# Performance work log

Measured on AMD Instinct MI355X. Metric: run time of the kernel, lower is better.

Reference implementation:

```python
import jax, jax.numpy as jnp
import numpy as np

B, S, HID = 2, 2048, 1024
NH = 16
DK = HID // NH


def setup_inputs() -> dict:
    key0 = jax.random.key(0)
    ks = jax.random.split(key0, 16)
    inp = {
        "query": jax.random.normal(ks[0], (B, S, HID), dtype=jnp.float32),
        "key": jax.random.normal(ks[1], (B, S, HID), dtype=jnp.float32),
        "value": jax.random.normal(ks[2], (B, S, HID), dtype=jnp.float32),
        "bias": jax.random.uniform(ks[3], (B, S), dtype=jnp.float32),
        "mask": jax.random.randint(ks[4], (B, 1, S), 0, 2, dtype=jnp.int32),
        "wq": jax.random.normal(ks[5], (HID, HID), dtype=jnp.float32) * 0.02,
        "bq": jax.random.normal(ks[6], (HID,), dtype=jnp.float32) * 0.02,
        "wk": jax.random.normal(ks[7], (HID, HID), dtype=jnp.float32) * 0.02,
        "bk": jax.random.normal(ks[8], (HID,), dtype=jnp.float32) * 0.02,
        "wv": jax.random.normal(ks[9], (HID, HID), dtype=jnp.float32) * 0.02,
        "bv": jax.random.normal(ks[10], (HID,), dtype=jnp.float32) * 0.02,
        "wo": jax.random.normal(ks[11], (HID, HID), dtype=jnp.float32) * 0.02,
        "bo": jax.random.normal(ks[12], (HID,), dtype=jnp.float32) * 0.02,
    }
    return inp


def reference(query, key, value, bias, mask, wq, bq, wk, bk, wv, bv, wo, bo):
    b, s, hid = query.shape
    # attn_bias_type == 'both': gate K and V with per-token scalar bias
    # (dropout is eval-mode identity): x + p[..., None] * x
    key = key + bias[:, :, None] * key
    value = value + bias[:, :, None] * value

    def proj(x, w, bb):
        # torch Linear: x @ W.T + b, then split heads -> [b, nh, s, dk]
        y = x @ w.T + bb
        return y.reshape(b, s, NH, DK).transpose(0, 2, 1, 3)

    q = proj(query, wq, bq)
    k = proj(key, wk, bk)
    v = proj(value, wv, bv)

    scores = jnp.einsum("bhqd,bhkd->bhqk", q, k) / jnp.sqrt(jnp.asarray(DK, q.dtype))
    m = mask[:, None]  # [b,1,1,s] broadcast over heads and query positions
    scores = jnp.where(m == 0, jnp.asarray(-10000.0, scores.dtype), scores)
    p_attn = jax.nn.softmax(scores, axis=-1)
    x = jnp.einsum("bhqk,bhkd->bhqd", p_attn, v)
    x = x.transpose(0, 2, 1, 3).reshape(b, s, hid)
    return x @ wo.T + bo
```

## Files before the change

### kernel.cpp

```cpp
#include <hip/hip_runtime.h>
#include <stdint.h>

#define NB   2
#define SS   2048
#define HIDN 1024
#define NHEAD 16
#define DKK  64

typedef __attribute__((ext_vector_type(8))) short bf16x8;
typedef __attribute__((ext_vector_type(4))) float f32x4;

__device__ __forceinline__ uint16_t f2bf(float f) {
    uint32_t u = __float_as_uint(f);
    u += 0x7FFF + ((u >> 16) & 1);
    return (uint16_t)(u >> 16);
}
__device__ __forceinline__ uint32_t pk2(float f0, float f1) {
    uint32_t u0 = __float_as_uint(f0);
    uint32_t u1 = __float_as_uint(f1);
    u0 += 0x7FFF + ((u0 >> 16) & 1);
    u1 += 0x7FFF + ((u1 >> 16) & 1);
    return (u0 >> 16) | (u1 & 0xFFFF0000u);
}
__device__ __forceinline__ uint4 pack8(const float* __restrict__ s, float sc) {
    float4 a = *(const float4*)s;
    float4 b = *(const float4*)(s + 4);
    uint4 r;
    r.x = pk2(sc * a.x, sc * a.y);
    r.y = pk2(sc * a.z, sc * a.w);
    r.z = pk2(sc * b.x, sc * b.y);
    r.w = pk2(sc * b.z, sc * b.w);
    return r;
}
__device__ __forceinline__ void gl_lds16(const uint16_t* g, uint16_t* l) {
    __builtin_amdgcn_global_load_lds((const __attribute__((address_space(1))) void*)g,
                                     (__attribute__((address_space(3))) void*)l,
                                     16, 0, 0);
}

__global__ __launch_bounds__(256, 4)
void cvt_all(const float* __restrict__ q, const float* __restrict__ k,
             const float* __restrict__ v, const float* __restrict__ bias,
             const float* __restrict__ w0, const float* __restrict__ w1,
             const float* __restrict__ w2, const float* __restrict__ w3,
             uint16_t* __restrict__ q16, uint16_t* __restrict__ k16,
             uint16_t* __restrict__ v16, uint16_t* __restrict__ w16o)
{
    int i = blockIdx.x * 256 + threadIdx.x;
    if (i < 524288) {
        size_t e = (size_t)i * 8;
        float sc = 1.0f + bias[i >> 7];
        *(uint4*)(q16 + e) = pack8(q + e, 1.0f);
        *(uint4*)(k16 + e) = pack8(k + e, sc);
        *(uint4*)(v16 + e) = pack8(v + e, sc);
    } else {
        int j = i - 524288;
        const float* src = (j < 131072) ? w0 : (j < 262144) ? w1
                         : (j < 393216) ? w2 : w3;
        size_t e = (size_t)(j & 131071) * 8;
        *(uint4*)(w16o + (size_t)(j >> 17) * 1048576 + e) = pack8(src + e, 1.0f);
    }
}

__device__ __forceinline__ void gemm_core(const uint16_t* __restrict__ A,
                                          const uint16_t* __restrict__ W,
                                          uint16_t* __restrict__ As0,
                                          uint16_t* __restrict__ As1,
                                          uint16_t* __restrict__ Bs0,
                                          uint16_t* __restrict__ Bs1,
                                          int m0, int n0,
                                          f32x4 acc[4][2])
{
    const int t    = threadIdx.x;
    const int w    = t >> 6;
    const int lane = t & 63;
    const int q    = lane >> 4;
    const int lr   = lane & 15;
    const int wr   = (w >> 1) * 64;
    const int wc   = (w & 1) * 32;
    const int srow = lane >> 3;
    const int sg   = (lane & 7) ^ srow;

#pragma unroll
    for (int c = 0; c < 4; ++c) {
        int r = w * 32 + c * 8;
        gl_lds16(A + (size_t)(m0 + r + srow) * HIDN + sg * 8, As0 + r * 64);
    }
#pragma unroll
    for (int c = 0; c < 2; ++c) {
        int r = w * 16 + c * 8;
        gl_lds16(W + (size_t)(n0 + r + srow) * HIDN + sg * 8, Bs0 + r * 64);
    }

    for (int it = 0; it < 16; ++it) {
        uint16_t* Asc = (it & 1) ? As1 : As0;
        uint16_t* Bsc = (it & 1) ? Bs1 : Bs0;
        uint16_t* Asn = (it & 1) ? As0 : As1;
        uint16_t* Bsn = (it & 1) ? Bs0 : Bs1;
        __syncthreads();
        if (it + 1 < 16) {
            int k0 = (it + 1) * 64;
#pragma unroll
            for (int c = 0; c < 4; ++c) {
                int r = w * 32 + c * 8;
                gl_lds16(A + (size_t)(m0 + r + srow) * HIDN + k0 + sg * 8,
                         Asn + r * 64);
            }
#pragma unroll
            for (int c = 0; c < 2; ++c) {
                int r = w * 16 + c * 8;
                gl_lds16(W + (size_t)(n0 + r + srow) * HIDN + k0 + sg * 8,
                         Bsn + r * 64);
            }
        }
        bf16x8 af[2][4], bfr[2][2];
#pragma unroll
        for (int s = 0; s < 2; ++s) {
#pragma unroll
            for (int i = 0; i < 4; ++i)
                af[s][i] = *(const bf16x8*)&Asc[(wr + i * 16 + lr) * 64 +
                                                (((s * 4 + q) ^ (lr & 7)) * 8)];
#pragma unroll
            for (int j = 0; j < 2; ++j)
                bfr[s][j] = *(const bf16x8*)&Bsc[(wc + j * 16 + lr) * 64 +
                                                 (((s * 4 + q) ^ (lr & 7)) * 8)];
        }
#pragma unroll
        for (int s = 0; s < 2; ++s)
#pragma unroll
            for (int i = 0; i < 4; ++i)
#pragma unroll
                for (int j = 0; j < 2; ++j)
                    acc[i][j] = __builtin_amdgcn_mfma_f32_16x16x32_bf16(
                        af[s][i], bfr[s][j], acc[i][j], 0, 0, 0);
    }
}

__global__ __launch_bounds__(256, 3)
void gemm_qkv(const uint16_t* __restrict__ Qin, const uint16_t* __restrict__ Kin,
              const uint16_t* __restrict__ Vin, const uint16_t* __restrict__ W16,
              const float* __restrict__ bq, const float* __restrict__ bk,
              const float* __restrict__ bv,
              uint16_t* __restrict__ Qb, uint16_t* __restrict__ Kb,
              uint16_t* __restrict__ Vtb)
{
    __shared__ __align__(16) uint16_t As[2][128 * 64];
    __shared__ __align__(16) uint16_t Bs[2][64 * 64];

    const int z = blockIdx.z;
    const uint16_t* A    = (z == 0) ? Qin : (z == 1) ? Kin : Vin;
    const uint16_t* W    = W16 + (size_t)z * 1048576;
    const float*    bias = (z == 0) ? bq : (z == 1) ? bk : bv;
    const float     osc  = (z == 0) ? 0.125f : 1.0f;

    const int t    = threadIdx.x;
    const int w    = t >> 6;
    const int lane = t & 63;
    const int q    = lane >> 4;
    const int lr   = lane & 15;
    const int wr   = (w >> 1) * 64;
    const int wc   = (w & 1) * 32;
    const int m0   = blockIdx.y * 128;
    const int n0   = blockIdx.x * 64;

    f32x4 acc[4][2] = {};
    gemm_core(A, W, As[0], As[1], Bs[0], Bs[1], m0, n0, acc);

    if (z < 2) {
        uint16_t* o = (z == 0) ? Qb : Kb;
#pragma unroll
        for (int i = 0; i < 4; ++i)
#pragma unroll
            for (int j = 0; j < 2; ++j) {
                int gn = n0 + wc + j * 16 + lr;
                float bvx = bias[gn];
#pragma unroll
                for (int r = 0; r < 4; ++r) {
                    int row = m0 + wr + i * 16 + q * 4 + r;
                    int b = row >> 11, s = row & 2047;
                    size_t dst = (size_t)b * (NHEAD * SS * DKK)
                               + (size_t)(gn >> 6) * (SS * DKK)
                               + (size_t)s * DKK + (gn & 63);
                    o[dst] = f2bf((acc[i][j][r] + bvx) * osc);
                }
            }
    } else {
        __syncthreads();
        uint16_t* Tr = (uint16_t*)As;
#pragma unroll
        for (int i = 0; i < 4; ++i)
#pragma unroll
            for (int j = 0; j < 2; ++j) {
                int d = wc + j * 16 + lr;
                float bvx = bias[n0 + d];
#pragma unroll
                for (int r = 0; r < 4; ++r) {
                    int sl = wr + i * 16 + q * 4 + r;
                    Tr[d * 136 + sl] = f2bf(acc[i][j][r] + bvx);
                }
            }
        __syncthreads();
        int b = m0 >> 11, h = n0 >> 6;
#pragma unroll
        for (int p = 0; p < 4; ++p) {
            int idx = p * 256 + t;
            int d   = idx >> 4;
            int sc8 = (idx & 15) * 8;
            size_t dst = ((size_t)(b * NHEAD + h) * DKK + d) * SS
                       + (m0 & 2047) + sc8;
            *(uint4*)&Vtb[dst] = *(const uint4*)&Tr[d * 136 + sc8];
        }
    }
}

__global__ __launch_bounds__(256, 3)
void gemm_out(const uint16_t* __restrict__ Xb, const uint16_t* __restrict__ W,
              const float* __restrict__ bias, float* __restrict__ out)
{
    __shared__ __align__(16) uint16_t As[2][128 * 64];
    __shared__ __align__(16) uint16_t Bs[2][64 * 64];

    const int t    = threadIdx.x;
    const int w    = t >> 6;
    const int lane = t & 63;
    const int q    = lane >> 4;
    const int lr   = lane & 15;
    const int wr   = (w >> 1) * 64;
    const int wc   = (w & 1) * 32;
    const int m0   = blockIdx.y * 128;
    const int n0   = blockIdx.x * 64;

    f32x4 acc[4][2] = {};
    gemm_core(Xb, W, As[0], As[1], Bs[0], Bs[1], m0, n0, acc);

#pragma unroll
    for (int i = 0; i < 4; ++i)
#pragma unroll
        for (int j = 0; j < 2; ++j) {
            int gn = n0 + wc + j * 16 + lr;
            float bvx = bias[gn];
#pragma unroll
            for (int r = 0; r < 4; ++r) {
                int row = m0 + wr + i * 16 + q * 4 + r;
                out[(size_t)row * HIDN + gn] = acc[i][j][r] + bvx;
            }
        }
}

__global__ __launch_bounds__(512, 4)
void flash_attn(const uint16_t* __restrict__ Qg, const uint16_t* __restrict__ Kg,
                const uint16_t* __restrict__ Vtg, const int* __restrict__ mask,
                uint16_t* __restrict__ X)
{
    __shared__ __align__(16) uint16_t QP[128 * 72];
    __shared__ __align__(16) uint16_t Ks[64 * 72];
    __shared__ __align__(16) uint16_t Vs[64 * 72];
    __shared__ __align__(16) float Amf[SS];

    const int t    = threadIdx.x;
    const int w    = t >> 6;
    const int lane = t & 63;
    const int q    = lane >> 4;
    const int lr   = lane & 15;
    const int bh   = blockIdx.y;
    const int b    = bh >> 4;
    const int h    = bh & 15;
    const int q0   = blockIdx.x * 128;
    const size_t head = (size_t)bh * SS * DKK;

#pragma unroll
    for (int p = 0; p < 2; ++p) {
        int idx = p * 512 + t;
        int row = idx >> 3;
        int col = (idx & 7) * 8;
        *(uint4*)&QP[row * 72 + col] =
            *(const uint4*)(Qg + head + (size_t)(q0 + row) * DKK + col);
    }
#pragma unroll
    for (int p = 0; p < 4; ++p) {
        int i = p * 512 + t;
        Amf[i] = (mask[b * SS + i] == 0) ? -10000.0f : 0.0f;
    }
    __syncthreads();

    bf16x8 qf[2];
#pragma unroll
    for (int s = 0; s < 2; ++s)
        qf[s] = *(const bf16x8*)&QP[(w * 16 + lr) * 72 + s * 32 + q * 8];

    float mst = -1e30f, lst = 0.0f;
    f32x4 oacc[4] = {};

    for (int kv0 = 0; kv0 < SS; kv0 += 64) {
        {
            int row = t >> 3;
            int col = (t & 7) * 8;
            *(uint4*)&Ks[row * 72 + col] =
                *(const uint4*)(Kg + head + (size_t)(kv0 + row) * DKK + col);
            *(uint4*)&Vs[row * 72 + col] =
                *(const uint4*)(Vtg + head + (size_t)row * SS + kv0 + col);
        }
        __syncthreads();

        f32x4 st[4];
#pragma unroll
        for (int ni = 0; ni < 4; ++ni) {
            bf16x8 kf0 = *(const bf16x8*)&Ks[(ni * 16 + lr) * 72 + 0  + q * 8];
            bf16x8 kf1 = *(const bf16x8*)&Ks[(ni * 16 + lr) * 72 + 32 + q * 8];
            f32x4 z = {0.0f, 0.0f, 0.0f, 0.0f};
            z = __builtin_amdgcn_mfma_f32_16x16x32_bf16(kf0, qf[0], z, 0, 0, 0);
            z = __builtin_amdgcn_mfma_f32_16x16x32_bf16(kf1, qf[1], z, 0, 0, 0);
            st[ni] = z;
        }

        float rmax = -1e30f;
#pragma unroll
        for (int ni = 0; ni < 4; ++ni) {
            float4 am = *(const float4*)&Amf[kv0 + ni * 16 + q * 4];
            st[ni][0] += am.x; st[ni][1] += am.y;
            st[ni][2] += am.z; st[ni][3] += am.w;
#pragma unroll
            for (int r = 0; r < 4; ++r) rmax = fmaxf(rmax, st[ni][r]);
        }
        rmax = fmaxf(rmax, __shfl_xor(rmax, 16));
        rmax = fmaxf(rmax, __shfl_xor(rmax, 32));

        float mnew  = fmaxf(mst, rmax);
        float alpha = __expf(mst - mnew);
        mst = mnew;

        float rsum = 0.0f;
#pragma unroll
        for (int ni = 0; ni < 4; ++ni) {
            float p0 = __expf(st[ni][0] - mst);
            float p1 = __expf(st[ni][1] - mst);
            float p2 = __expf(st[ni][2] - mst);
            float p3 = __expf(st[ni][3] - mst);
            rsum += (p0 + p1) + (p2 + p3);
            uint2 pw = make_uint2(pk2(p0, p1), pk2(p2, p3));
            *(uint2*)&QP[(w * 16 + lr) * 72 + ni * 16 + q * 4] = pw;
        }
        rsum += __shfl_xor(rsum, 16);
        rsum += __shfl_xor(rsum, 32);
        lst = lst * alpha + rsum;
#pragma unroll
        for (int dj = 0; dj < 4; ++dj) {
            oacc[dj][0] *= alpha; oacc[dj][1] *= alpha;
            oacc[dj][2] *= alpha; oacc[dj][3] *= alpha;
        }

#pragma unroll
        for (int ks = 0; ks < 2; ++ks) {
            bf16x8 pfB = *(const bf16x8*)&QP[(w * 16 + lr) * 72 + ks * 32 + q * 8];
#pragma unroll
            for (int dj = 0; dj < 4; ++dj) {
                bf16x8 vfA = *(const bf16x8*)&Vs[(dj * 16 + lr) * 72 + ks * 32 + q * 8];
                oacc[dj] = __builtin_amdgcn_mfma_f32_16x16x32_bf16(vfA, pfB, oacc[dj], 0, 0, 0);
            }
        }
        __syncthreads();
    }

    {
        float inv = 1.0f / lst;
        int s = q0 + w * 16 + lr;
        uint16_t* xp = X + (size_t)(b * SS + s) * HIDN + h * DKK;
#pragma unroll
        for (int dj = 0; dj < 4; ++dj) {
            uint2 pw = make_uint2(pk2(oacc[dj][0] * inv, oacc[dj][1] * inv),
                                  pk2(oacc[dj][2] * inv, oacc[dj][3] * inv));
            *(uint2*)(xp + dj * 16 + q * 4) = pw;
        }
    }
}

extern "C" void kernel_launch(void* const* d_in, const int* in_sizes, int n_in,
                              void* d_out, int out_size, void* d_ws, size_t ws_size,
                              hipStream_t stream) {
    const float* query = (const float*)d_in[0];
    const float* key   = (const float*)d_in[1];
    const float* value = (const float*)d_in[2];
    const float* bias  = (const float*)d_in[3];
    const int*   mask  = (const int*)d_in[4];
    const float* wq = (const float*)d_in[5];
    const float* bq = (const float*)d_in[6];
    const float* wk = (const float*)d_in[7];
    const float* bk = (const float*)d_in[8];
    const float* wv = (const float*)d_in[9];
    const float* bv = (const float*)d_in[10];
    const float* wo = (const float*)d_in[11];
    const float* bo = (const float*)d_in[12];

    const size_t TEN = (size_t)NB * SS * HIDN;
    uint16_t* Qin = (uint16_t*)d_ws;
    uint16_t* Kin = Qin + TEN;
    uint16_t* Vin = Kin + TEN;
    uint16_t* W16 = Vin + TEN;
    uint16_t* Qb  = W16 + 4 * 1048576;
    uint16_t* Kb  = Qb + TEN;
    uint16_t* Vtb = Kb + TEN;
    uint16_t* Xb  = Qin;

    cvt_all<<<4096, 256, 0, stream>>>(query, key, value, bias,
                                      wq, wk, wv, wo, Qin, Kin, Vin, W16);
    gemm_qkv<<<dim3(16, 32, 3), 256, 0, stream>>>(Qin, Kin, Vin, W16,
                                                  bq, bk, bv, Qb, Kb, Vtb);
    flash_attn<<<dim3(SS / 128, NB * NHEAD), 512, 0, stream>>>(Qb, Kb, Vtb, mask, Xb);
    gemm_out<<<dim3(16, 32), 256, 0, stream>>>(Xb, W16 + 3 * 1048576, bo, (float*)d_out);
}
```

Baseline: 252.6 us.

## Prefetch K/V tiles into registers and use exp2 softmax with lazy rescale

The attention kernel now loads the next K/V tile into registers while the current tile is being processed, overlapping global loads with MFMA work. The softmax switches to base-2 exponentials: log2(e) is folded into the Q projection scale and the mask constant, and v_exp_f32 is used directly. The running max and rescale of the accumulators are updated only when the new row max exceeds the old one by a threshold, which skips the alpha multiply on most iterations. Bf16 packing uses the hardware v_cvt_pk_bf16_f32 instruction. These changes add register pressure and allow bounded growth in the exponent range before a rescale.

```diff
diff --git a/kernel.cpp b/kernel.cpp
--- a/kernel.cpp
+++ b/kernel.cpp
@@ -21,6 +21,16 @@
     u0 += 0x7FFF + ((u0 >> 16) & 1);
     u1 += 0x7FFF + ((u1 >> 16) & 1);
     return (u0 >> 16) | (u1 & 0xFFFF0000u);
+}
+__device__ __forceinline__ uint32_t cvtpk(float lo, float hi) {
+    uint32_t r;
+    asm("v_cvt_pk_bf16_f32 %0, %1, %2" : "=v"(r) : "v"(lo), "v"(hi));
+    return r;
+}
+__device__ __forceinline__ float exp2_fast(float x) {
+    float r;
+    asm("v_exp_f32 %0, %1" : "=v"(r) : "v"(x));
+    return r;
 }
 __device__ __forceinline__ uint4 pack8(const float* __restrict__ s, float sc) {
     float4 a = *(const float4*)s;
@@ -151,7 +161,7 @@
     const uint16_t* A    = (z == 0) ? Qin : (z == 1) ? Kin : Vin;
     const uint16_t* W    = W16 + (size_t)z * 1048576;
     const float*    bias = (z == 0) ? bq : (z == 1) ? bk : bv;
-    const float     osc  = (z == 0) ? 0.125f : 1.0f;
+    const float     osc  = (z == 0) ? 0.125f * 1.44269504f : 1.0f;
 
     const int t    = threadIdx.x;
     const int w    = t >> 6;
@@ -279,8 +289,14 @@
 #pragma unroll
     for (int p = 0; p < 4; ++p) {
         int i = p * 512 + t;
-        Amf[i] = (mask[b * SS + i] == 0) ? -10000.0f : 0.0f;
-    }
+        Amf[i] = (mask[b * SS + i] == 0) ? -14426.95f : 0.0f;
+    }
+
+    const int srow = t >> 3;
+    const int scol = (t & 7) * 8;
+    uint4 kreg = *(const uint4*)(Kg + head + (size_t)srow * DKK + scol);
+    uint4 vreg = *(const uint4*)(Vtg + head + (size_t)srow * SS + scol);
+
     __syncthreads();
 
     bf16x8 qf[2];
@@ -292,15 +308,14 @@
     f32x4 oacc[4] = {};
 
     for (int kv0 = 0; kv0 < SS; kv0 += 64) {
-        {
-            int row = t >> 3;
-            int col = (t & 7) * 8;
-            *(uint4*)&Ks[row * 72 + col] =
-                *(const uint4*)(Kg + head + (size_t)(kv0 + row) * DKK + col);
-            *(uint4*)&Vs[row * 72 + col] =
-                *(const uint4*)(Vtg + head + (size_t)row * SS + kv0 + col);
-        }
+        *(uint4*)&Ks[srow * 72 + scol] = kreg;
+        *(uint4*)&Vs[srow * 72 + scol] = vreg;
         __syncthreads();
+
+        if (kv0 + 64 < SS) {
+            kreg = *(const uint4*)(Kg + head + (size_t)(kv0 + 64 + srow) * DKK + scol);
+            vreg = *(const uint4*)(Vtg + head + (size_t)srow * SS + kv0 + 64 + scol);
+        }
 
         f32x4 st[4];
 #pragma unroll
@@ -325,29 +340,32 @@
         rmax = fmaxf(rmax, __shfl_xor(rmax, 16));
         rmax = fmaxf(rmax, __shfl_xor(rmax, 32));
 
-        float mnew  = fmaxf(mst, rmax);
-        float alpha = __expf(mst - mnew);
-        mst = mnew;
+        if (__any(rmax > mst + 11.5f)) {
+            float mnew  = fmaxf(mst, rmax);
+            float alpha = exp2_fast(mst - mnew);
+            mst = mnew;
+            lst *= alpha;
+#pragma unroll
+            for (int dj = 0; dj < 4; ++dj) {
+                oacc[dj][0] *= alpha; oacc[dj][1] *= alpha;
+                oacc[dj][2] *= alpha; oacc[dj][3] *= alpha;
+            }
+        }
 
         float rsum = 0.0f;
 #pragma unroll
         for (int ni = 0; ni < 4; ++ni) {
-            float p0 = __expf(st[ni][0] - mst);
-            float p1 = __expf(st[ni][1] - mst);
-            float p2 = __expf(st[ni][2] - mst);
-            float p3 = __expf(st[ni][3] - mst);
+            float p0 = exp2_fast(st[ni][0] - mst);
+            float p1 = exp2_fast(st[ni][1] - mst);
+            float p2 = exp2_fast(st[ni][2] - mst);
+            float p3 = exp2_fast(st[ni][3] - mst);
             rsum += (p0 + p1) + (p2 + p3);
-            uint2 pw = make_uint2(pk2(p0, p1), pk2(p2, p3));
+            uint2 pw = make_uint2(cvtpk(p0, p1), cvtpk(p2, p3));
             *(uint2*)&QP[(w * 16 + lr) * 72 + ni * 16 + q * 4] = pw;
         }
         rsum += __shfl_xor(rsum, 16);
         rsum += __shfl_xor(rsum, 32);
-        lst = lst * alpha + rsum;
-#pragma unroll
-        for (int dj = 0; dj < 4; ++dj) {
-            oacc[dj][0] *= alpha; oacc[dj][1] *= alpha;
-            oacc[dj][2] *= alpha; oacc[dj][3] *= alpha;
-        }
+        lst += rsum;
 
 #pragma unroll
         for (int ks = 0; ks < 2; ++ks) {
@@ -367,8 +385,8 @@
         uint16_t* xp = X + (size_t)(b * SS + s) * HIDN + h * DKK;
 #pragma unroll
         for (int dj = 0; dj < 4; ++dj) {
-            uint2 pw = make_uint2(pk2(oacc[dj][0] * inv, oacc[dj][1] * inv),
-                                  pk2(oacc[dj][2] * inv, oacc[dj][3] * inv));
+            uint2 pw = make_uint2(cvtpk(oacc[dj][0] * inv, oacc[dj][1] * inv),
+                                  cvtpk(oacc[dj][2] * inv, oacc[dj][3] * inv));
             *(uint2*)(xp + dj * 16 + q * 4) = pw;
         }
     }
```

Measured after the change: 250.2 us. Within noise of the previous version (-0.9%).
